# Performance work log

Measured on AMD Instinct MI355X. Metric: run time of the kernel, lower is better.

Reference implementation:

```python
import jax, jax.numpy as jnp
import numpy as np

TAU = 0.25
VTH = 1.0
RESET = 0.0


def setup_inputs() -> dict:
    key = jax.random.key(0)
    B, T, U = 64, 256, 1024
    inputs = jax.random.normal(key, (B, T, U), dtype=jnp.float32)
    return {"inputs": inputs}


def reference(inputs):
    # inputs: (B, T, U). LIF recurrence over time with threshold + soft reset.
    dt = inputs.dtype
    tau = jnp.asarray(TAU, dt)
    vth = jnp.asarray(VTH, dt)
    reset = jnp.asarray(RESET, dt)

    def step(v, x_t):
        v = tau * v + (1.0 - tau) * x_t          # leaky integrate
        s = (v > vth).astype(dt)                  # fire
        v = v - s * vth + s * reset               # reset fired neurons
        return v, s

    B, T, U = inputs.shape
    v0 = jnp.zeros((B, U), dtype=dt)
    xs = jnp.swapaxes(inputs, 0, 1)               # (T, B, U)
    _, spikes = jax.lax.scan(step, v0, xs)        # (T, B, U)
    return jnp.swapaxes(spikes, 0, 1)             # (B, T, U)
```

## Files before the change

kernel.cpp:

```cpp
#include <hip/hip_runtime.h>
#include <hip/hip_bf16.h>


typedef float vfloat4 __attribute__((ext_vector_type(4)));

constexpr int kB = 64;
constexpr int kT = 256;
constexpr int kU = 1024;
constexpr int kG = 16;
constexpr int kPad = 72;

__global__ __launch_bounds__(256)
void lif_kernel(const float* __restrict__ x, float* __restrict__ out) {
    const int idx  = blockIdx.x * blockDim.x + threadIdx.x;
    const int b    = idx >> 10;
    const int u    = idx & (kU - 1);
    const int lane = threadIdx.x & 63;
    const int wav  = threadIdx.x >> 6;

    const size_t base = (size_t)b * kT * kU + u;
    const float* __restrict__ xp = x + base;
    const int ubase = u - lane;
    const size_t obase = (size_t)b * kT * kU + ubase;

    __shared__ float tile[4][kG][kPad];
    float (*T)[kPad] = tile[wav];

    float buf[kG], nbuf[kG];
#pragma unroll
    for (int j = 0; j < kG; ++j)
        buf[j] = xp[(size_t)j * kU];

    float v = 0.0f;
    for (int g = 0; g < kT / kG; ++g) {
        const int t0 = g * kG;
        const bool more = (g + 1 < kT / kG);
        if (more) {
#pragma unroll
            for (int j = 0; j < kG; ++j)
                nbuf[j] = xp[(size_t)(t0 + kG + j) * kU];
        }
#pragma unroll
        for (int j = 0; j < kG; ++j) {
            const float a  = __fmul_rn(0.25f, v);
            const float cc = __fmul_rn(0.75f, buf[j]);
            v = __fadd_rn(a, cc);
            const float s = (v > 1.0f) ? 1.0f : 0.0f;
            v = __fsub_rn(v, s);
            T[j][lane] = s;
        }
#pragma unroll
        for (int p = 0; p < 4; ++p) {
            const int tt  = lane & 15;
            const int grp = (lane >> 4) + 4 * p;
            const vfloat4 w = *(const vfloat4*)&T[tt][grp * 4];
            __builtin_nontemporal_store(
                w, (vfloat4*)&out[obase + (size_t)(t0 + tt) * kU + grp * 4]);
        }
        if (more) {
#pragma unroll
            for (int j = 0; j < kG; ++j)
                buf[j] = nbuf[j];
        }
    }
}

extern "C" void kernel_launch(void* const* d_in, const int* in_sizes, int n_in,
                              void* d_out, int out_size, void* d_ws, size_t ws_size,
                              hipStream_t stream) {
    const float* x = (const float*)d_in[0];
    float* out = (float*)d_out;

    const int nthreads = kB * kU;
    const int block = 256;
    const int grid = nthreads / block;
    lif_kernel<<<grid, block, 0, stream>>>(x, out);
}
```

Measured before the change: 113.1 us.

## Split LIF into bit-packed spike pass and separate float expansion kernel

```diff
diff --git a/kernel.cpp b/kernel.cpp
--- a/kernel.cpp
+++ b/kernel.cpp
@@ -8,23 +8,79 @@
 constexpr int kT = 256;
 constexpr int kU = 1024;
 constexpr int kG = 16;
-constexpr int kPad = 72;
 
 __global__ __launch_bounds__(256)
-void lif_kernel(const float* __restrict__ x, float* __restrict__ out) {
+void lif_pack(const float* __restrict__ x, unsigned long long* __restrict__ ws) {
     const int idx  = blockIdx.x * blockDim.x + threadIdx.x;
     const int b    = idx >> 10;
     const int u    = idx & (kU - 1);
     const int lane = threadIdx.x & 63;
-    const int wav  = threadIdx.x >> 6;
+    const int u64i = u >> 6;
 
+    const float* __restrict__ xp = x + (size_t)b * kT * kU + u;
+    unsigned long long* __restrict__ wp = ws + ((size_t)b * 16 + u64i) * kT;
+
+    float buf[kG], nbuf[kG];
+#pragma unroll
+    for (int j = 0; j < kG; ++j)
+        buf[j] = xp[(size_t)j * kU];
+
+    float v = 0.0f;
+    unsigned long long myMask = 0;
+    for (int g = 0; g < kT / kG; ++g) {
+        const int t0 = g * kG;
+        const bool more = (g + 1 < kT / kG);
+        if (more) {
+#pragma unroll
+            for (int j = 0; j < kG; ++j)
+                nbuf[j] = xp[(size_t)(t0 + kG + j) * kU];
+        }
+#pragma unroll
+        for (int j = 0; j < kG; ++j) {
+            const float a  = __fmul_rn(0.25f, v);
+            const float cc = __fmul_rn(0.75f, buf[j]);
+            v = __fadd_rn(a, cc);
+            const bool pred = (v > 1.0f);
+            v = __fsub_rn(v, pred ? 1.0f : 0.0f);
+            const unsigned long long m = __ballot(pred);
+            if (lane == ((t0 + j) & 63)) myMask = m;
+        }
+        if ((g & 3) == 3) {
+            wp[(g >> 2) * 64 + lane] = myMask;
+        }
+        if (more) {
+#pragma unroll
+            for (int j = 0; j < kG; ++j)
+                buf[j] = nbuf[j];
+        }
+    }
+}
+
+__global__ __launch_bounds__(256)
+void lif_expand(const unsigned long long* __restrict__ ws, vfloat4* __restrict__ out) {
+    const int f  = blockIdx.x * blockDim.x + threadIdx.x;
+    const int u4 = f & 255;
+    const int t  = (f >> 8) & 255;
+    const int b  = f >> 16;
+
+    const unsigned long long w = ws[((size_t)b * 16 + (u4 >> 4)) * kT + t];
+    const unsigned s = (unsigned)(w >> ((u4 & 15) * 4)) & 0xFu;
+    vfloat4 o;
+    o.x = (s & 1u) ? 1.0f : 0.0f;
+    o.y = (s & 2u) ? 1.0f : 0.0f;
+    o.z = (s & 4u) ? 1.0f : 0.0f;
+    o.w = (s & 8u) ? 1.0f : 0.0f;
+    out[f] = o;
+}
+
+__global__ __launch_bounds__(256)
+void lif_kernel(const float* __restrict__ x, float* __restrict__ out) {
+    const int idx = blockIdx.x * blockDim.x + threadIdx.x;
+    const int b = idx >> 10;
+    const int u = idx & (kU - 1);
     const size_t base = (size_t)b * kT * kU + u;
     const float* __restrict__ xp = x + base;
-    const int ubase = u - lane;
-    const size_t obase = (size_t)b * kT * kU + ubase;
-
-    __shared__ float tile[4][kG][kPad];
-    float (*T)[kPad] = tile[wav];
+    float* __restrict__ op = out + base;
 
     float buf[kG], nbuf[kG];
 #pragma unroll
@@ -47,15 +103,7 @@
             v = __fadd_rn(a, cc);
             const float s = (v > 1.0f) ? 1.0f : 0.0f;
             v = __fsub_rn(v, s);
-            T[j][lane] = s;
-        }
-#pragma unroll
-        for (int p = 0; p < 4; ++p) {
-            const int tt  = lane & 15;
-            const int grp = (lane >> 4) + 4 * p;
-            const vfloat4 w = *(const vfloat4*)&T[tt][grp * 4];
-            __builtin_nontemporal_store(
-                w, (vfloat4*)&out[obase + (size_t)(t0 + tt) * kU + grp * 4]);
+            op[(size_t)(t0 + j) * kU] = s;
         }
         if (more) {
 #pragma unroll
@@ -69,10 +117,13 @@
                               void* d_out, int out_size, void* d_ws, size_t ws_size,
                               hipStream_t stream) {
     const float* x = (const float*)d_in[0];
-    float* out = (float*)d_out;
+    const size_t packedBytes = (size_t)kB * kT * kU / 8;
 
-    const int nthreads = kB * kU;
-    const int block = 256;
-    const int grid = nthreads / block;
-    lif_kernel<<<grid, block, 0, stream>>>(x, out);
+    if (ws_size >= packedBytes) {
+        unsigned long long* ws = (unsigned long long*)d_ws;
+        lif_pack<<<kB * kU / 256, 256, 0, stream>>>(x, ws);
+        lif_expand<<<kB * kT * kU / 4 / 256, 256, 0, stream>>>(ws, (vfloat4*)d_out);
+    } else {
+        lif_kernel<<<kB * kU / 256, 256, 0, stream>>>(x, (float*)d_out);
+    }
 }
```

After: 122.9 us. 1.09x slower.
